# Kernel tuning notes

Measured on AMD Instinct MI355X. Metric: run time of the kernel, lower is better.

Reference implementation:

```python
import jax, jax.numpy as jnp
import numpy as np

B, L = 2048, 64          # sentence pairs, leaves per balanced binary tree
V, IN, M, HID, NC = 50000, 300, 150, 50, 5


def setup_inputs() -> dict:
    key = jax.random.key(0)
    ks = jax.random.split(key, 16)
    lin = lambda k, fi, fo: jax.random.normal(k, (fi, fo), jnp.float32) / np.sqrt(fi).astype(np.float32)
    bias = lambda k, fo: jax.random.normal(k, (fo,), jnp.float32) * 0.01
    return {
        "ltokens": jax.random.randint(ks[0], (B, L), 0, V, dtype=jnp.int32),
        "rtokens": jax.random.randint(ks[1], (B, L), 0, V, dtype=jnp.int32),
        "emb":   jax.random.normal(ks[2], (V, IN), jnp.float32),
        "Wioux": lin(ks[3], IN, 3 * M), "bioux": bias(ks[4], 3 * M),
        "Wiouh": lin(ks[5], M, 3 * M), "biouh": bias(ks[6], 3 * M),
        "Wfx":   lin(ks[7], IN, M),    "bfx":   bias(ks[8], M),
        "Wfh":   lin(ks[9], M, M),     "bfh":   bias(ks[10], M),
        "Wh":    lin(ks[11], 2 * M, HID), "bh": bias(ks[12], HID),
        "Wp":    lin(ks[13], HID, NC),    "bp": bias(ks[14], NC),
    }


def _split_iou(iou, m):
    return iou[..., :m], iou[..., m:2 * m], iou[..., 2 * m:]


def _encode(tokens, emb, Wioux, bioux, Wiouh, biouh, Wfh, bfh):
    m = Wfh.shape[0]
    x = emb[tokens]                                   # [B, L, IN]
    # Leaves: child_h = child_c = 0, so iouh contributes only its bias and fc = 0.
    iou = x @ Wioux + bioux + biouh                   # [B, L, 3M]
    i, o, u = _split_iou(iou, m)
    c = jax.nn.sigmoid(i) * jnp.tanh(u)
    h = jax.nn.sigmoid(o) * jnp.tanh(c)
    # Internal nodes level by level (inputs=None branch of node_forward).
    while h.shape[1] > 1:
        Bq, n, _ = h.shape
        ch = h.reshape(Bq, n // 2, 2, m)              # children h
        cc = c.reshape(Bq, n // 2, 2, m)              # children c
        iou = ch.sum(axis=2) @ Wiouh + biouh          # child-sum
        i, o, u = _split_iou(iou, m)
        f = jax.nn.sigmoid(ch @ Wfh + bfh)            # per-child forget gate
        c = jax.nn.sigmoid(i) * jnp.tanh(u) + (f * cc).sum(axis=2)
        h = jax.nn.sigmoid(o) * jnp.tanh(c)
    # ROOT in the original just passes its single child's state through.
    return h[:, 0]                                    # [B, M]


def reference(ltokens, rtokens, emb, Wioux, bioux, Wiouh, biouh, Wfx, bfx, Wfh, bfh, Wh, bh, Wp, bp):
    lh = _encode(ltokens, emb, Wioux, bioux, Wiouh, biouh, Wfh, bfh)
    rh = _encode(rtokens, emb, Wioux, bioux, Wiouh, biouh, Wfh, bfh)
    vec = jnp.concatenate([lh * rh, jnp.abs(lh - rh)], axis=-1)   # [B, 2M]
    mid = jax.nn.sigmoid(vec @ Wh + bh)
    return jax.nn.log_softmax(mid @ Wp + bp, axis=-1)             # [B, NC]
```

## Files before the change

kernel.cpp:

```cpp
#include <hip/hip_runtime.h>
#include <hip/hip_bf16.h>
#include <math.h>

constexpr int B_   = 2048;
constexpr int L_   = 64;
constexpr int V_   = 50000;
constexpr int IN_  = 300;
constexpr int M_   = 150;
constexpr int HID_ = 50;
constexpr int NC_  = 5;

constexpr int KP_  = 160;
constexpr int GN_  = 608;
constexpr int GNT_ = 19;
constexpr int GKC_ = 5;
constexpr int GCH_ = GN_ * 32;
constexpr int GQS_ = GN_ * 8;
constexpr int LEAF_N  = 480;
constexpr int LEAF_NT = 15;
constexpr int LEAF_KC = 10;
constexpr int LEAF_CH = LEAF_N * 32;
constexpr int LEAF_QS = LEAF_N * 8;

typedef float f32x4  __attribute__((ext_vector_type(4)));
typedef short bf16x8 __attribute__((ext_vector_type(8)));
typedef short short4v __attribute__((ext_vector_type(4)));

__device__ __forceinline__ float rcp_f(float x) { return __builtin_amdgcn_rcpf(x); }
__device__ __forceinline__ float sgm(float x)   { return rcp_f(1.0f + __expf(-x)); }
__device__ __forceinline__ float tanh_f(float x){ return 1.0f - 2.0f * rcp_f(1.0f + __expf(2.0f * x)); }

__device__ __forceinline__ short f2bs(float f) {
    union { __hip_bfloat16 h; short s; } u; u.h = __float2bfloat16(f); return u.s;
}
__device__ __forceinline__ float bs2f(short s) {
    union { short s; __hip_bfloat16 h; } u; u.s = s; return __bfloat162float(u.h);
}

__device__ __forceinline__ void gl_lds16(const short* g, short* l) {
    __builtin_amdgcn_global_load_lds(
        (const __attribute__((address_space(1))) unsigned int*)g,
        (__attribute__((address_space(3))) unsigned int*)l, 16, 0, 0);
}

__global__ __launch_bounds__(256) void prep_kernel(
    const float* __restrict__ Wioux, const float* __restrict__ Wiouh,
    const float* __restrict__ Wfh, short* __restrict__ Bg, short* __restrict__ Bx)
{
    const int tid = blockIdx.x * blockDim.x + threadIdx.x;
    const int nthr = gridDim.x * blockDim.x;
    const int tot1 = GKC_ * GCH_;
    for (int idx = tid; idx < tot1; idx += nthr) {
        const int kc = idx / GCH_;
        int rem = idx % GCH_;
        const int q = rem / GQS_; rem %= GQS_;
        const int n = rem / 8, j = rem % 8;
        const int k = kc * 32 + q * 8 + j;
        const int m = n >> 2, g = n & 3;
        float v = 0.0f;
        if (k < M_ && m < M_)
            v = (g < 3) ? Wiouh[k * 450 + g * 150 + m] : Wfh[k * M_ + m];
        Bg[idx] = f2bs(v);
    }
    const int tot2 = LEAF_KC * LEAF_CH;
    for (int idx = tid; idx < tot2; idx += nthr) {
        const int kc = idx / LEAF_CH;
        int rem = idx % LEAF_CH;
        const int q = rem / LEAF_QS; rem %= LEAF_QS;
        const int n = rem / 8, j = rem % 8;
        const int k = kc * 32 + q * 8 + j;
        float v = (k < IN_ && n < 450) ? Wioux[k * 450 + n] : 0.0f;
        Bx[idx] = f2bs(v);
    }
}

__global__ __launch_bounds__(512) void leaf_gemm(
    const float* __restrict__ emb, const short* __restrict__ Bx,
    const float* __restrict__ bioux, const float* __restrict__ biouh,
    short* __restrict__ LeafH, short* __restrict__ LeafC)
{
    __shared__ __align__(16) char smem[LEAF_CH * 2 + 64 * 64];
    short* Bs = (short*)smem;
    short* As = (short*)(smem + LEAF_CH * 2);
    float* Es = (float*)smem;

    const int t = threadIdx.x;
    const int row0 = blockIdx.x * 64;
    const int w = t >> 6, lane = t & 63;
    const int mt = w & 3, nt0 = (w >> 2) * LEAF_NT;
    const int lr = lane & 15, quad = lane >> 4;

    f32x4 acc[LEAF_NT];
    #pragma unroll
    for (int i = 0; i < LEAF_NT; i++) { acc[i][0] = 0; acc[i][1] = 0; acc[i][2] = 0; acc[i][3] = 0; }

    const int arow = t >> 3, apart = t & 7;
    const int av = row0 + arow;
    const int aq = apart >> 1, aj = (apart & 1) * 4;

    for (int kc = 0; kc < LEAF_KC; kc++) {
        const short* bsrc = Bx + (size_t)kc * LEAF_CH;
        #pragma unroll
        for (int i = 0; i < 3; i++)
            gl_lds16(bsrc + (i * 512 + t) * 8, Bs + (i * 512 + (t & ~63)) * 8);
        if (t < 384)
            gl_lds16(bsrc + (1536 + t) * 8, Bs + (1536 + (t & ~63)) * 8);
        {
            const int k0 = kc * 32 + apart * 4;
            float4 x = make_float4(0.f, 0.f, 0.f, 0.f);
            if (av < V_ && k0 < IN_) x = *(const float4*)&emb[(size_t)av * IN_ + k0];
            short4v s;
            s[0] = f2bs(x.x); s[1] = f2bs(x.y); s[2] = f2bs(x.z); s[3] = f2bs(x.w);
            *(short4v*)&As[aq * 512 + arow * 8 + aj] = s;
        }
        __syncthreads();
        bf16x8 a = *(const bf16x8*)&As[quad * 512 + (mt * 16 + lr) * 8];
        #pragma unroll
        for (int i = 0; i < LEAF_NT; i++) {
            bf16x8 b = *(const bf16x8*)&Bs[quad * LEAF_QS + ((nt0 + i) * 16 + lr) * 8];
            acc[i] = __builtin_amdgcn_mfma_f32_16x16x32_bf16(a, b, acc[i], 0, 0, 0);
        }
        __syncthreads();
    }

    for (int mc = 0; mc < 4; mc++) {
        if (mt == mc) {
            #pragma unroll
            for (int i = 0; i < LEAF_NT; i++) {
                const int col = (nt0 + i) * 16 + lr;
                #pragma unroll
                for (int r = 0; r < 4; r++) Es[(quad * 4 + r) * LEAF_N + col] = acc[i][r];
            }
        }
        __syncthreads();
        for (int p = t; p < 16 * KP_; p += 512) {
            const int rl = p / KP_, n = p % KP_;
            const int v = row0 + mc * 16 + rl;
            if (v < V_) {
                if (n < M_) {
                    const float i_ = Es[rl * LEAF_N + n]       + bioux[n]       + biouh[n];
                    const float o_ = Es[rl * LEAF_N + n + 150] + bioux[n + 150] + biouh[n + 150];
                    const float u_ = Es[rl * LEAF_N + n + 300] + bioux[n + 300] + biouh[n + 300];
                    const float c = sgm(i_) * tanh_f(u_);
                    const float h = sgm(o_) * tanh_f(c);
                    LeafH[(size_t)v * KP_ + n] = f2bs(h);
                    LeafC[(size_t)v * KP_ + n] = f2bs(c);
                } else {
                    LeafH[(size_t)v * KP_ + n] = 0;
                    LeafC[(size_t)v * KP_ + n] = 0;
                }
            }
        }
        __syncthreads();
    }
}

__global__ __launch_bounds__(512) void leafGF_gemm(
    const short* __restrict__ LeafH, const short* __restrict__ LeafC,
    const short* __restrict__ Bg, const float* __restrict__ bfh,
    short* __restrict__ LeafE)
{
    __shared__ __align__(16) char smem[GCH_ * 2 + 4096 + KP_ * 64 * 2 + 600];
    short* Bs   = (short*)smem;
    short* As   = (short*)(smem + GCH_ * 2);
    short* CinS = (short*)(smem + GCH_ * 2 + 4096);
    float* bfs  = (float*)(smem + GCH_ * 2 + 4096 + KP_ * 64 * 2);
    short* Os = Bs;

    const int t = threadIdx.x;
    const int v0 = blockIdx.x * 64;
    const int w = t >> 6, lane = t & 63;
    const int mt = w & 3, nt0 = (w >> 2) * GNT_;
    const int lr = lane & 15, quad = lane >> 4;
    const int c = lane & 15;

    if (t < 150) bfs[t] = bfh[t];
    const short* csrc = LeafC + (size_t)v0 * KP_;
    #pragma unroll
    for (int i = 0; i < 2; i++)
        gl_lds16(csrc + (i * 512 + t) * 8, CinS + (i * 512 + (t & ~63)) * 8);
    if (t < 256)
        gl_lds16(csrc + (1024 + t) * 8, CinS + (1024 + (t & ~63)) * 8);

    f32x4 acc[GNT_];
    #pragma unroll
    for (int i = 0; i < GNT_; i++) { acc[i][0] = 0; acc[i][1] = 0; acc[i][2] = 0; acc[i][3] = 0; }

    const int arow = t & 63, apart = t >> 6;
    const size_t srow = (size_t)((v0 + arow < V_) ? (v0 + arow) : 0);
    const short* asrc = LeafH + srow * KP_ + apart * 8;

    for (int kc = 0; kc < GKC_; kc++) {
        const short* bsrc = Bg + (size_t)kc * GCH_;
        #pragma unroll
        for (int i = 0; i < 4; i++)
            gl_lds16(bsrc + (i * 512 + t) * 8, Bs + (i * 512 + (t & ~63)) * 8);
        if (t < 384)
            gl_lds16(bsrc + (2048 + t) * 8, Bs + (2048 + (t & ~63)) * 8);
        if (t < 256)
            gl_lds16(asrc + kc * 32, As + (t & ~63) * 8);
        __syncthreads();
        bf16x8 a = *(const bf16x8*)&As[quad * 512 + (mt * 16 + lr) * 8];
        #pragma unroll
        for (int i = 0; i < GNT_; i++) {
            bf16x8 b = *(const bf16x8*)&Bs[quad * GQS_ + ((nt0 + i) * 16 + lr) * 8];
            acc[i] = __builtin_amdgcn_mfma_f32_16x16x32_bf16(a, b, acc[i], 0, 0, 0);
        }
        __syncthreads();
    }

    for (int ph = 0; ph < 2; ph++) {
        if ((mt >> 1) == ph) {
            const int rbase = 16 * (mt & 1) + 4 * quad;
            #pragma unroll
            for (int i = 0; i < GNT_; i++) {
                const int col = (nt0 + i) * 16 + c;
                const int m = col >> 2, g = col & 3;
                #pragma unroll
                for (int r = 0; r < 4; r++) {
                    short ov;
                    if (g == 3) {
                        if (m < M_) {
                            const float cc = bs2f(CinS[(32 * ph + rbase + r) * KP_ + m]);
                            ov = f2bs(sgm(acc[i][r] + bfs[m]) * cc);
                        } else ov = 0;
                    } else ov = f2bs(acc[i][r]);
                    Os[(rbase + r) * GN_ + col] = ov;
                }
            }
        }
        __syncthreads();
        const int vb = v0 + 32 * ph;
        const int4* os4 = (const int4*)Os;
        for (int u = t; u < 2432; u += 512) {
            const int row = u / 76;
            if (vb + row < V_)
                ((int4*)(LeafE + (size_t)(vb + row) * GN_))[u - row * 76] = os4[u];
        }
        __syncthreads();
    }
}

template<int CS>
__device__ __forceinline__ void level_epilogue(
    const f32x4* acc, int mt, int nt0, int lane,
    const short* CinS, const float* bias_s, short* Hs, short* Cs)
{
    const int q = lane >> 4, c = lane & 15, g = c & 3, lb = lane & ~3;
    #pragma unroll
    for (int i = 0; i < GNT_; i++) {
        const int col = (nt0 + i) * 16 + c;
        const int m = col >> 2;
        const float vA = acc[i][0] + acc[i][1];
        const float vB = acc[i][2] + acc[i][3];
        const float iA = __shfl(vA, lb), oA = __shfl(vA, lb + 1), uA = __shfl(vA, lb + 2);
        const float iB = __shfl(vB, lb), oB = __shfl(vB, lb + 1), uB = __shfl(vB, lb + 2);
        const float fA0 = __shfl(acc[i][0], lb + 3), fA1 = __shfl(acc[i][1], lb + 3);
        const float fB0 = __shfl(acc[i][2], lb + 3), fB1 = __shfl(acc[i][3], lb + 3);
        if (g < 2 && m < M_) {
            const float iv = g ? iB : iA, ov = g ? oB : oA, uv = g ? uB : uA;
            const float fl = g ? fB0 : fA0, fr = g ? fB1 : fA1;
            const int node = 8 * mt + 2 * q + g;
            const int ch = 16 * mt + 4 * q + 2 * g;
            const float cl = bs2f(CinS[ch * CS + m]);
            const float cr = bs2f(CinS[(ch + 1) * CS + m]);
            const float bf = bias_s[450 + m];
            const float cv = sgm(iv + bias_s[m]) * tanh_f(uv + bias_s[m + 300])
                           + sgm(fl + bf) * cl + sgm(fr + bf) * cr;
            const float hv = sgm(ov + bias_s[m + 150]) * tanh_f(cv);
            Hs[node * KP_ + m] = f2bs(hv);
            Cs[node * KP_ + m] = f2bs(cv);
        }
    }
}

__global__ __launch_bounds__(512) void level1_fused(
    const int* __restrict__ ltok, const int* __restrict__ rtok,
    const short* __restrict__ LeafE, const short* __restrict__ Bg,
    const float* __restrict__ biouh, const float* __restrict__ bfh,
    short* __restrict__ Hout, short* __restrict__ Cout)
{
    constexpr int CS1 = 152;
    __shared__ __align__(16) char smem[GCH_ * 2 + 20480 + 64 * CS1 * 2 + 2400];
    short* Bs     = (short*)smem;
    short* AsF    = (short*)(smem + GCH_ * 2);
    short* CinS   = (short*)(smem + GCH_ * 2 + 20480);
    float* bias_s = (float*)(smem + GCH_ * 2 + 20480 + 64 * CS1 * 2);
    short* Hs = Bs;
    short* Cs = Bs + 32 * KP_;

    const int t = threadIdx.x;
    const int out0 = blockIdx.x * 32;
    const int w = t >> 6, lane = t & 63;
    const int mt = w & 3, nt0 = (w >> 2) * GNT_;
    const int lr = lane & 15, quad = lane >> 4;

    if (t < 600) bias_s[t] = (t < 450) ? biouh[t] : bfh[t - 450];
    __syncthreads();

    {
        const int row = t >> 3, qs = t & 7;
        const int gidx = blockIdx.x * 128 + 2 * row;
        const int* tsrc = (gidx < B_ * L_) ? (ltok + gidx) : (rtok + gidx - B_ * L_);
        const short* el = LeafE + (size_t)tsrc[0] * GN_;
        const short* er = LeafE + (size_t)tsrc[1] * GN_;
        #pragma unroll
        for (int s = 0; s < 5; s++) {
            const int Q = qs + 8 * s;
            short4v hq = {0, 0, 0, 0}, cq = {0, 0, 0, 0};
            if (Q < 38) {
                union { int4 v[2]; short s16[16]; } ue, ur;
                ue.v[0] = *(const int4*)(el + Q * 16);
                ue.v[1] = *(const int4*)(el + Q * 16 + 8);
                ur.v[0] = *(const int4*)(er + Q * 16);
                ur.v[1] = *(const int4*)(er + Q * 16 + 8);
                #pragma unroll
                for (int jj = 0; jj < 4; jj++) {
                    const int m = 4 * Q + jj;
                    if (m < M_) {
                        const float i_ = bs2f(ue.s16[4 * jj])     + bs2f(ur.s16[4 * jj])     + bias_s[m];
                        const float o_ = bs2f(ue.s16[4 * jj + 1]) + bs2f(ur.s16[4 * jj + 1]) + bias_s[m + 150];
                        const float u_ = bs2f(ue.s16[4 * jj + 2]) + bs2f(ur.s16[4 * jj + 2]) + bias_s[m + 300];
                        const float fc = bs2f(ue.s16[4 * jj + 3]) + bs2f(ur.s16[4 * jj + 3]);
                        const float cv = sgm(i_) * tanh_f(u_) + fc;
                        const float hv = sgm(o_) * tanh_f(cv);
                        hq[jj] = f2bs(hv); cq[jj] = f2bs(cv);
                    }
                }
            }
            const int m0 = 4 * Q;
            const int kc = m0 >> 5, q = (m0 >> 3) & 3, j0 = m0 & 7;
            *(short4v*)&AsF[(kc * 4 + q) * 512 + row * 8 + j0] = hq;
            *(short4v*)&CinS[row * CS1 + m0] = cq;
        }
    }

    f32x4 acc[GNT_];
    #pragma unroll
    for (int i = 0; i < GNT_; i++) { acc[i][0] = 0; acc[i][1] = 0; acc[i][2] = 0; acc[i][3] = 0; }

    for (int kc = 0; kc < GKC_; kc++) {
        const short* bsrc = Bg + (size_t)kc * GCH_;
        #pragma unroll
        for (int i = 0; i < 4; i++)
            gl_lds16(bsrc + (i * 512 + t) * 8, Bs + (i * 512 + (t & ~63)) * 8);
        if (t < 384)
            gl_lds16(bsrc + (2048 + t) * 8, Bs + (2048 + (t & ~63)) * 8);
        __syncthreads();
        bf16x8 a = *(const bf16x8*)&AsF[kc * 2048 + quad * 512 + (mt * 16 + lr) * 8];
        #pragma unroll
        for (int i = 0; i < GNT_; i++) {
            bf16x8 b = *(const bf16x8*)&Bs[quad * GQS_ + ((nt0 + i) * 16 + lr) * 8];
            acc[i] = __builtin_amdgcn_mfma_f32_16x16x32_bf16(a, b, acc[i], 0, 0, 0);
        }
        __syncthreads();
    }

    if (t < 320) { const int node = t / 10, mm = 150 + t % 10;
                   Hs[node * KP_ + mm] = 0; Cs[node * KP_ + mm] = 0; }
    level_epilogue<CS1>(acc, mt, nt0, lane, CinS, bias_s, Hs, Cs);
    __syncthreads();
    int4* Hg = (int4*)(Hout + (size_t)out0 * KP_);
    int4* Cg = (int4*)(Cout + (size_t)out0 * KP_);
    const int4* hs4 = (const int4*)Hs;
    const int4* cs4 = (const int4*)Cs;
    for (int u = t; u < 1280; u += 512) {
        if (u < 640) Hg[u] = hs4[u]; else Cg[u - 640] = cs4[u - 640];
    }
}

__global__ __launch_bounds__(512) void level_gemm(
    const short* __restrict__ Hin, const short* __restrict__ Cin,
    const short* __restrict__ Bg,
    const float* __restrict__ biouh, const float* __restrict__ bfh,
    short* __restrict__ Hout, short* __restrict__ Cout)
{
    __shared__ __align__(16) char smem[GCH_ * 2 + 4096 + 20480 + 2400];
    short* Bs     = (short*)smem;
    short* As     = (short*)(smem + GCH_ * 2);
    short* CinS   = (short*)(smem + GCH_ * 2 + 4096);
    float* bias_s = (float*)(smem + GCH_ * 2 + 4096 + 20480);
    short* Hs = Bs;
    short* Cs = Bs + 32 * KP_;

    const int t = threadIdx.x;
    const int row0 = blockIdx.x * 64, out0 = blockIdx.x * 32;
    const int w = t >> 6, lane = t & 63;
    const int mt = w & 3, nt0 = (w >> 2) * GNT_;
    const int lr = lane & 15, quad = lane >> 4;

    if (t < 600) bias_s[t] = (t < 450) ? biouh[t] : bfh[t - 450];
    const short* csrc = Cin + (size_t)row0 * KP_;
    #pragma unroll
    for (int i = 0; i < 2; i++)
        gl_lds16(csrc + (i * 512 + t) * 8, CinS + (i * 512 + (t & ~63)) * 8);
    if (t < 256)
        gl_lds16(csrc + (1024 + t) * 8, CinS + (1024 + (t & ~63)) * 8);

    f32x4 acc[GNT_];
    #pragma unroll
    for (int i = 0; i < GNT_; i++) { acc[i][0] = 0; acc[i][1] = 0; acc[i][2] = 0; acc[i][3] = 0; }

    const short* asrc = Hin + (size_t)(row0 + (t & 63)) * KP_ + (t >> 6) * 8;

    for (int kc = 0; kc < GKC_; kc++) {
        const short* bsrc = Bg + (size_t)kc * GCH_;
        #pragma unroll
        for (int i = 0; i < 4; i++)
            gl_lds16(bsrc + (i * 512 + t) * 8, Bs + (i * 512 + (t & ~63)) * 8);
        if (t < 384)
            gl_lds16(bsrc + (2048 + t) * 8, Bs + (2048 + (t & ~63)) * 8);
        if (t < 256)
            gl_lds16(asrc + kc * 32, As + (t & ~63) * 8);
        __syncthreads();
        bf16x8 a = *(const bf16x8*)&As[quad * 512 + (mt * 16 + lr) * 8];
        #pragma unroll
        for (int i = 0; i < GNT_; i++) {
            bf16x8 b = *(const bf16x8*)&Bs[quad * GQS_ + ((nt0 + i) * 16 + lr) * 8];
            acc[i] = __builtin_amdgcn_mfma_f32_16x16x32_bf16(a, b, acc[i], 0, 0, 0);
        }
        __syncthreads();
    }

    if (t < 320) { const int node = t / 10, mm = 150 + t % 10;
                   Hs[node * KP_ + mm] = 0; Cs[node * KP_ + mm] = 0; }
    level_epilogue<KP_>(acc, mt, nt0, lane, CinS, bias_s, Hs, Cs);
    __syncthreads();
    int4* Hg = (int4*)(Hout + (size_t)out0 * KP_);
    int4* Cg = (int4*)(Cout + (size_t)out0 * KP_);
    const int4* hs4 = (const int4*)Hs;
    const int4* cs4 = (const int4*)Cs;
    for (int u = t; u < 1280; u += 512) {
        if (u < 640) Hg[u] = hs4[u]; else Cg[u - 640] = cs4[u - 640];
    }
}

__global__ __launch_bounds__(64) void head_kernel(
    const short* __restrict__ RootH,
    const float* __restrict__ Wh, const float* __restrict__ bh,
    const float* __restrict__ Wp, const float* __restrict__ bp,
    float* __restrict__ out)
{
    __shared__ float vec[2 * M_];
    __shared__ float mid[HID_];
    __shared__ float lg[NC_];
    __shared__ float lse;

    const int b = blockIdx.x;
    const int t = threadIdx.x;
    const short* lh = RootH + (size_t)b * KP_;
    const short* rh = RootH + (size_t)(B_ + b) * KP_;

    for (int i = t; i < M_; i += 64) {
        const float a = bs2f(lh[i]), c = bs2f(rh[i]);
        vec[i]      = a * c;
        vec[M_ + i] = fabsf(a - c);
    }
    __syncthreads();

    for (int j = t; j < HID_; j += 64) {
        float acc = bh[j];
        for (int k = 0; k < 2 * M_; k++) acc += vec[k] * Wh[k * HID_ + j];
        mid[j] = sgm(acc);
    }
    __syncthreads();

    if (t < NC_) {
        float acc = bp[t];
        for (int k = 0; k < HID_; k++) acc += mid[k] * Wp[k * NC_ + t];
        lg[t] = acc;
    }
    __syncthreads();

    if (t == 0) {
        float mx = lg[0];
        for (int i = 1; i < NC_; i++) mx = fmaxf(mx, lg[i]);
        float s = 0.0f;
        for (int i = 0; i < NC_; i++) s += expf(lg[i] - mx);
        lse = mx + logf(s);
    }
    __syncthreads();

    if (t < NC_) out[b * NC_ + t] = lg[t] - lse;
}

extern "C" void kernel_launch(void* const* d_in, const int* in_sizes, int n_in,
                              void* d_out, int out_size, void* d_ws, size_t ws_size,
                              hipStream_t stream)
{
    const int*   ltok  = (const int*)d_in[0];
    const int*   rtok  = (const int*)d_in[1];
    const float* emb   = (const float*)d_in[2];
    const float* Wioux = (const float*)d_in[3];
    const float* bioux = (const float*)d_in[4];
    const float* Wiouh = (const float*)d_in[5];
    const float* biouh = (const float*)d_in[6];
    const float* Wfh   = (const float*)d_in[9];
    const float* bfh   = (const float*)d_in[10];
    const float* Wh    = (const float*)d_in[11];
    const float* bh    = (const float*)d_in[12];
    const float* Wp    = (const float*)d_in[13];
    const float* bp    = (const float*)d_in[14];
    float* out = (float*)d_out;

    char* ws = (char*)d_ws;
    size_t off = 0;
    auto carve = [&](size_t bytes) { char* p = ws + off; off += (bytes + 255) & ~(size_t)255; return p; };
    short* Bg    = (short*)carve((size_t)GKC_ * GCH_ * 2);
    short* Bx    = (short*)carve((size_t)LEAF_KC * LEAF_CH * 2);
    short* LeafH = (short*)carve((size_t)V_ * KP_ * 2);
    short* LeafC = (short*)carve((size_t)V_ * KP_ * 2);
    short* LeafE = (short*)carve((size_t)V_ * GN_ * 2);
    short* HA    = (short*)carve((size_t)65536 * KP_ * 2);
    short* CA    = (short*)carve((size_t)65536 * KP_ * 2);
    short* HB    = (short*)carve((size_t)32768 * KP_ * 2);
    short* CB    = (short*)carve((size_t)32768 * KP_ * 2);

    hipLaunchKernelGGL(prep_kernel, dim3(128), dim3(256), 0, stream, Wioux, Wiouh, Wfh, Bg, Bx);
    hipLaunchKernelGGL(leaf_gemm, dim3((V_ + 63) / 64), dim3(512), 0, stream,
                       emb, Bx, bioux, biouh, LeafH, LeafC);
    hipLaunchKernelGGL(leafGF_gemm, dim3((V_ + 63) / 64), dim3(512), 0, stream,
                       LeafH, LeafC, Bg, bfh, LeafE);
    hipLaunchKernelGGL(level1_fused, dim3(2048), dim3(512), 0, stream,
                       ltok, rtok, LeafE, Bg, biouh, bfh, HA, CA);
    hipLaunchKernelGGL(level_gemm, dim3(1024), dim3(512), 0, stream,
                       HA, CA, Bg, biouh, bfh, HB, CB);
    hipLaunchKernelGGL(level_gemm, dim3(512), dim3(512), 0, stream,
                       HB, CB, Bg, biouh, bfh, HA, CA);
    hipLaunchKernelGGL(level_gemm, dim3(256), dim3(512), 0, stream,
                       HA, CA, Bg, biouh, bfh, HB, CB);
    hipLaunchKernelGGL(level_gemm, dim3(128), dim3(512), 0, stream,
                       HB, CB, Bg, biouh, bfh, HA, CA);
    hipLaunchKernelGGL(head_kernel, dim3(B_), dim3(64), 0, stream, HA, Wh, bh, Wp, bp, out);
}
```

Measured before the change: 532.2 us.

## Replace per-vocab gate precompute with gathered leaf-level GEMM

Removes the leafGF_gemm pass, which precomputed per-vocabulary iou/forget-gate products into a wide 608-column LeafE table that level 1 then gathered. Adds a level0_gemm that gathers the 160-column LeafH/LeafC rows by token directly into LDS and runs the child-sum GEMM over all 131072 leaves; level 1 becomes an ordinary level_gemm. The intent is to cut gather traffic and the large intermediate table. The cost is more MFMA work, since the leaf level now runs over all gathered leaves instead of the 50000 vocabulary rows. Workspace buffers are reused, with HA aliased onto LeafH.

```diff
diff --git a/kernel.cpp b/kernel.cpp
--- a/kernel.cpp
+++ b/kernel.cpp
@@ -150,92 +150,6 @@
                     LeafC[(size_t)v * KP_ + n] = 0;
                 }
             }
-        }
-        __syncthreads();
-    }
-}
-
-__global__ __launch_bounds__(512) void leafGF_gemm(
-    const short* __restrict__ LeafH, const short* __restrict__ LeafC,
-    const short* __restrict__ Bg, const float* __restrict__ bfh,
-    short* __restrict__ LeafE)
-{
-    __shared__ __align__(16) char smem[GCH_ * 2 + 4096 + KP_ * 64 * 2 + 600];
-    short* Bs   = (short*)smem;
-    short* As   = (short*)(smem + GCH_ * 2);
-    short* CinS = (short*)(smem + GCH_ * 2 + 4096);
-    float* bfs  = (float*)(smem + GCH_ * 2 + 4096 + KP_ * 64 * 2);
-    short* Os = Bs;
-
-    const int t = threadIdx.x;
-    const int v0 = blockIdx.x * 64;
-    const int w = t >> 6, lane = t & 63;
-    const int mt = w & 3, nt0 = (w >> 2) * GNT_;
-    const int lr = lane & 15, quad = lane >> 4;
-    const int c = lane & 15;
-
-    if (t < 150) bfs[t] = bfh[t];
-    const short* csrc = LeafC + (size_t)v0 * KP_;
-    #pragma unroll
-    for (int i = 0; i < 2; i++)
-        gl_lds16(csrc + (i * 512 + t) * 8, CinS + (i * 512 + (t & ~63)) * 8);
-    if (t < 256)
-        gl_lds16(csrc + (1024 + t) * 8, CinS + (1024 + (t & ~63)) * 8);
-
-    f32x4 acc[GNT_];
-    #pragma unroll
-    for (int i = 0; i < GNT_; i++) { acc[i][0] = 0; acc[i][1] = 0; acc[i][2] = 0; acc[i][3] = 0; }
-
-    const int arow = t & 63, apart = t >> 6;
-    const size_t srow = (size_t)((v0 + arow < V_) ? (v0 + arow) : 0);
-    const short* asrc = LeafH + srow * KP_ + apart * 8;
-
-    for (int kc = 0; kc < GKC_; kc++) {
-        const short* bsrc = Bg + (size_t)kc * GCH_;
-        #pragma unroll
-        for (int i = 0; i < 4; i++)
-            gl_lds16(bsrc + (i * 512 + t) * 8, Bs + (i * 512 + (t & ~63)) * 8);
-        if (t < 384)
-            gl_lds16(bsrc + (2048 + t) * 8, Bs + (2048 + (t & ~63)) * 8);
-        if (t < 256)
-            gl_lds16(asrc + kc * 32, As + (t & ~63) * 8);
-        __syncthreads();
-        bf16x8 a = *(const bf16x8*)&As[quad * 512 + (mt * 16 + lr) * 8];
-        #pragma unroll
-        for (int i = 0; i < GNT_; i++) {
-            bf16x8 b = *(const bf16x8*)&Bs[quad * GQS_ + ((nt0 + i) * 16 + lr) * 8];
-            acc[i] = __builtin_amdgcn_mfma_f32_16x16x32_bf16(a, b, acc[i], 0, 0, 0);
-        }
-        __syncthreads();
-    }
-
-    for (int ph = 0; ph < 2; ph++) {
-        if ((mt >> 1) == ph) {
-            const int rbase = 16 * (mt & 1) + 4 * quad;
-            #pragma unroll
-            for (int i = 0; i < GNT_; i++) {
-                const int col = (nt0 + i) * 16 + c;
-                const int m = col >> 2, g = col & 3;
-                #pragma unroll
-                for (int r = 0; r < 4; r++) {
-                    short ov;
-                    if (g == 3) {
-                        if (m < M_) {
-                            const float cc = bs2f(CinS[(32 * ph + rbase + r) * KP_ + m]);
-                            ov = f2bs(sgm(acc[i][r] + bfs[m]) * cc);
-                        } else ov = 0;
-                    } else ov = f2bs(acc[i][r]);
-                    Os[(rbase + r) * GN_ + col] = ov;
-                }
-            }
-        }
-        __syncthreads();
-        const int vb = v0 + 32 * ph;
-        const int4* os4 = (const int4*)Os;
-        for (int u = t; u < 2432; u += 512) {
-            const int row = u / 76;
-            if (vb + row < V_)
-                ((int4*)(LeafE + (size_t)(vb + row) * GN_))[u - row * 76] = os4[u];
         }
         __syncthreads();
     }
@@ -274,18 +188,19 @@
     }
 }
 
-__global__ __launch_bounds__(512) void level1_fused(
+__global__ __launch_bounds__(512, 4) void level0_gemm(
     const int* __restrict__ ltok, const int* __restrict__ rtok,
-    const short* __restrict__ LeafE, const short* __restrict__ Bg,
+    const short* __restrict__ LeafH, const short* __restrict__ LeafC,
+    const short* __restrict__ Bg,
     const float* __restrict__ biouh, const float* __restrict__ bfh,
     short* __restrict__ Hout, short* __restrict__ Cout)
 {
-    constexpr int CS1 = 152;
-    __shared__ __align__(16) char smem[GCH_ * 2 + 20480 + 64 * CS1 * 2 + 2400];
+    __shared__ __align__(16) char smem[GCH_ * 2 + 4096 + 20480 + 2400 + 256];
     short* Bs     = (short*)smem;
-    short* AsF    = (short*)(smem + GCH_ * 2);
-    short* CinS   = (short*)(smem + GCH_ * 2 + 20480);
-    float* bias_s = (float*)(smem + GCH_ * 2 + 20480 + 64 * CS1 * 2);
+    short* As     = (short*)(smem + GCH_ * 2);
+    short* CinS   = (short*)(smem + GCH_ * 2 + 4096);
+    float* bias_s = (float*)(smem + GCH_ * 2 + 4096 + 20480);
+    int*   toks   = (int*)(smem + GCH_ * 2 + 4096 + 20480 + 2400);
     short* Hs = Bs;
     short* Cs = Bs + 32 * KP_;
 
@@ -296,48 +211,23 @@
     const int lr = lane & 15, quad = lane >> 4;
 
     if (t < 600) bias_s[t] = (t < 450) ? biouh[t] : bfh[t - 450];
-    __syncthreads();
-
-    {
-        const int row = t >> 3, qs = t & 7;
-        const int gidx = blockIdx.x * 128 + 2 * row;
-        const int* tsrc = (gidx < B_ * L_) ? (ltok + gidx) : (rtok + gidx - B_ * L_);
-        const short* el = LeafE + (size_t)tsrc[0] * GN_;
-        const short* er = LeafE + (size_t)tsrc[1] * GN_;
-        #pragma unroll
-        for (int s = 0; s < 5; s++) {
-            const int Q = qs + 8 * s;
-            short4v hq = {0, 0, 0, 0}, cq = {0, 0, 0, 0};
-            if (Q < 38) {
-                union { int4 v[2]; short s16[16]; } ue, ur;
-                ue.v[0] = *(const int4*)(el + Q * 16);
-                ue.v[1] = *(const int4*)(el + Q * 16 + 8);
-                ur.v[0] = *(const int4*)(er + Q * 16);
-                ur.v[1] = *(const int4*)(er + Q * 16 + 8);
-                #pragma unroll
-                for (int jj = 0; jj < 4; jj++) {
-                    const int m = 4 * Q + jj;
-                    if (m < M_) {
-                        const float i_ = bs2f(ue.s16[4 * jj])     + bs2f(ur.s16[4 * jj])     + bias_s[m];
-                        const float o_ = bs2f(ue.s16[4 * jj + 1]) + bs2f(ur.s16[4 * jj + 1]) + bias_s[m + 150];
-                        const float u_ = bs2f(ue.s16[4 * jj + 2]) + bs2f(ur.s16[4 * jj + 2]) + bias_s[m + 300];
-                        const float fc = bs2f(ue.s16[4 * jj + 3]) + bs2f(ur.s16[4 * jj + 3]);
-                        const float cv = sgm(i_) * tanh_f(u_) + fc;
-                        const float hv = sgm(o_) * tanh_f(cv);
-                        hq[jj] = f2bs(hv); cq[jj] = f2bs(cv);
-                    }
-                }
-            }
-            const int m0 = 4 * Q;
-            const int kc = m0 >> 5, q = (m0 >> 3) & 3, j0 = m0 & 7;
-            *(short4v*)&AsF[(kc * 4 + q) * 512 + row * 8 + j0] = hq;
-            *(short4v*)&CinS[row * CS1 + m0] = cq;
-        }
+    if (t < 64) {
+        const int g = blockIdx.x * 64 + t;
+        toks[t] = (g < B_ * L_) ? ltok[g] : rtok[g - B_ * L_];
+    }
+    __syncthreads();
+
+    for (int u = t; u < 1280; u += 512) {
+        const int row = u / 20, part = u - row * 20;
+        gl_lds16(LeafC + (size_t)toks[row] * KP_ + part * 8,
+                 CinS + (u & ~63) * 8);
     }
 
     f32x4 acc[GNT_];
     #pragma unroll
     for (int i = 0; i < GNT_; i++) { acc[i][0] = 0; acc[i][1] = 0; acc[i][2] = 0; acc[i][3] = 0; }
+
+    const short* abase = LeafH + (size_t)toks[t & 63] * KP_ + (t >> 6) * 8;
 
     for (int kc = 0; kc < GKC_; kc++) {
         const short* bsrc = Bg + (size_t)kc * GCH_;
@@ -346,8 +236,10 @@
             gl_lds16(bsrc + (i * 512 + t) * 8, Bs + (i * 512 + (t & ~63)) * 8);
         if (t < 384)
             gl_lds16(bsrc + (2048 + t) * 8, Bs + (2048 + (t & ~63)) * 8);
-        __syncthreads();
-        bf16x8 a = *(const bf16x8*)&AsF[kc * 2048 + quad * 512 + (mt * 16 + lr) * 8];
+        if (t < 256)
+            gl_lds16(abase + kc * 32, As + (t & ~63) * 8);
+        __syncthreads();
+        bf16x8 a = *(const bf16x8*)&As[quad * 512 + (mt * 16 + lr) * 8];
         #pragma unroll
         for (int i = 0; i < GNT_; i++) {
             bf16x8 b = *(const bf16x8*)&Bs[quad * GQS_ + ((nt0 + i) * 16 + lr) * 8];
@@ -358,7 +250,7 @@
 
     if (t < 320) { const int node = t / 10, mm = 150 + t % 10;
                    Hs[node * KP_ + mm] = 0; Cs[node * KP_ + mm] = 0; }
-    level_epilogue<CS1>(acc, mt, nt0, lane, CinS, bias_s, Hs, Cs);
+    level_epilogue<KP_>(acc, mt, nt0, lane, CinS, bias_s, Hs, Cs);
     __syncthreads();
     int4* Hg = (int4*)(Hout + (size_t)out0 * KP_);
     int4* Cg = (int4*)(Cout + (size_t)out0 * KP_);
@@ -510,19 +402,20 @@
     short* Bx    = (short*)carve((size_t)LEAF_KC * LEAF_CH * 2);
     short* LeafH = (short*)carve((size_t)V_ * KP_ * 2);
     short* LeafC = (short*)carve((size_t)V_ * KP_ * 2);
-    short* LeafE = (short*)carve((size_t)V_ * GN_ * 2);
-    short* HA    = (short*)carve((size_t)65536 * KP_ * 2);
+    short* H0    = (short*)carve((size_t)131072 * KP_ * 2);
+    short* C0    = (short*)carve((size_t)131072 * KP_ * 2);
     short* CA    = (short*)carve((size_t)65536 * KP_ * 2);
-    short* HB    = (short*)carve((size_t)32768 * KP_ * 2);
-    short* CB    = (short*)carve((size_t)32768 * KP_ * 2);
+    short* HA = LeafH;
+    short* HB = H0;
+    short* CB = C0;
 
     hipLaunchKernelGGL(prep_kernel, dim3(128), dim3(256), 0, stream, Wioux, Wiouh, Wfh, Bg, Bx);
     hipLaunchKernelGGL(leaf_gemm, dim3((V_ + 63) / 64), dim3(512), 0, stream,
                        emb, Bx, bioux, biouh, LeafH, LeafC);
-    hipLaunchKernelGGL(leafGF_gemm, dim3((V_ + 63) / 64), dim3(512), 0, stream,
-                       LeafH, LeafC, Bg, bfh, LeafE);
-    hipLaunchKernelGGL(level1_fused, dim3(2048), dim3(512), 0, stream,
-                       ltok, rtok, LeafE, Bg, biouh, bfh, HA, CA);
+    hipLaunchKernelGGL(level0_gemm, dim3(4096), dim3(512), 0, stream,
+                       ltok, rtok, LeafH, LeafC, Bg, biouh, bfh, H0, C0);
+    hipLaunchKernelGGL(level_gemm, dim3(2048), dim3(512), 0, stream,
+                       H0, C0, Bg, biouh, bfh, HA, CA);
     hipLaunchKernelGGL(level_gemm, dim3(1024), dim3(512), 0, stream,
                        HA, CA, Bg, biouh, bfh, HB, CB);
     hipLaunchKernelGGL(level_gemm, dim3(512), dim3(512), 0, stream,
```

Result: slower. 587.2 us (+10.3%).
